# Kernel tuning notes

Measured on AMD Instinct MI355X. Metric: run time of the kernel, lower is better.

Reference implementation:

```python
import jax, jax.numpy as jnp
import numpy as np

L, B = 1024, 64
VALID_FRAC = 0.9  # fraction of residues with nonzero (observed) coordinates in y


def setup_inputs() -> dict:
    key = jax.random.key(0)
    kx, ky = jax.random.split(key)
    x = jax.random.normal(kx, (L, B, 3), dtype=jnp.float32)
    y = jax.random.normal(ky, (L, B, 3), dtype=jnp.float32)
    # zero out trailing residues in y so the dynamic mask (co.sum() != 0) is exercised
    valid = (jnp.arange(L) < int(VALID_FRAC * L))[:, None, None]
    y = y * valid.astype(jnp.float32)
    return {"x": x, "y": y}


def _masked_pair_dist(pts, pair_mask):
    # pts: [B, L, 3]; pair_mask: [B, L, L] (False on diagonal and on padded rows/cols)
    sq = jnp.sum(pts * pts, axis=-1)                                   # [B, L]
    d2 = sq[:, :, None] + sq[:, None, :] - 2.0 * jnp.einsum('bld,bmd->blm', pts, pts)
    d2 = jnp.maximum(d2, 0.0)                                          # relu, matches F.relu
    safe = jnp.where(pair_mask, d2, 1.0)                               # keep sqrt grad finite
    return jnp.where(pair_mask, jnp.sqrt(safe), 0.0)


def reference(x, y):
    # x, y: [L, B, 3] -> permute to [B, L, 3] as in the torch module
    xb = jnp.transpose(x, (1, 0, 2))
    yb = jnp.transpose(y, (1, 0, 2))
    Bn, Ln = xb.shape[0], xb.shape[1]
    # mask: residues of y whose coordinate sum is nonzero (index_select in original)
    mask = (jnp.sum(yb, axis=-1) != 0)                                 # [B, L]
    off_diag = ~jnp.eye(Ln, dtype=bool)
    pair_mask = mask[:, :, None] & mask[:, None, :] & off_diag         # [B, L, L]
    xd = _masked_pair_dist(xb, pair_mask)
    yd = _masked_pair_dist(yb, pair_mask)
    D = yd - xd                                                        # [B, L, L]
    per_batch = jnp.sqrt(jnp.sum(D * D, axis=(1, 2)))                  # Frobenius norm per batch
    denom = (Ln ** 2 / 2 - Ln) ** 0.5                                  # x.size(1)**2/2 - x.size(1)
    out = jnp.sum(per_batch) / denom / Bn
    return out.reshape(1)
```

## Files before the change

### kernel.cpp

```cpp
#include <hip/hip_runtime.h>
#include <math.h>

#define Lp 1024
#define Bp 64
#define Tt 128
#define NTILE 8
#define NPAIR 36

typedef float v2 __attribute__((ext_vector_type(2)));
static __device__ __forceinline__ v2 splat2(float s) { v2 r; r.x = s; r.y = s; return r; }
static __device__ __forceinline__ v2 lo2(float4 v)   { v2 r; r.x = v.x; r.y = v.y; return r; }
static __device__ __forceinline__ v2 hi2(float4 v)   { v2 r; r.x = v.z; r.y = v.w; return r; }

__global__ __launch_bounds__(256) void drmsd_main(
    const float* __restrict__ x, const float* __restrict__ y,
    float* __restrict__ partials, float* __restrict__ moments)
{
    __shared__ __align__(16) float xsx[2][Tt], xsy[2][Tt], xsz[2][Tt];
    __shared__ __align__(16) float ysx[2][Tt], ysy[2][Tt], ysz[2][Tt];
    __shared__ __align__(16) float ms[2][Tt];
    __shared__ float red[4];
    __shared__ float mred[4][9];

    const int b = blockIdx.x;
    const int p = blockIdx.y;
    const int t = threadIdx.x;

    int ti = 0, base = 0;
    while (p >= base + (NTILE - ti)) { base += (NTILE - ti); ++ti; }
    const int tj = ti + (p - base);

    {
        const int r     = t & (Tt - 1);
        const int which = t >> 7;
        const int tile  = which ? tj : ti;
        const int row   = tile * Tt + r;
        const float* px = x + (size_t)row * (Bp * 3) + (size_t)b * 3;
        const float* py = y + (size_t)row * (Bp * 3) + (size_t)b * 3;
        const float x0 = px[0], x1 = px[1], x2 = px[2];
        const float y0 = py[0], y1 = py[1], y2 = py[2];
        xsx[which][r] = x0; xsy[which][r] = x1; xsz[which][r] = x2;
        ysx[which][r] = y0; ysy[which][r] = y1; ysz[which][r] = y2;
        ms[which][r]  = ((y0 + y1 + y2) != 0.0f) ? 1.0f : 0.0f;
    }
    __syncthreads();

    const int jc = (t & 15) << 2;
    const int rg = t >> 4;

    float4 jxx[2], jxy[2], jxz[2], jyx[2], jyy[2], jyz[2], jm4[2];
#pragma unroll
    for (int jj = 0; jj < 2; ++jj) {
        const int j0 = jj * 64 + jc;
        jxx[jj] = *(const float4*)&xsx[1][j0];
        jxy[jj] = *(const float4*)&xsy[1][j0];
        jxz[jj] = *(const float4*)&xsz[1][j0];
        jyx[jj] = *(const float4*)&ysx[1][j0];
        jyy[jj] = *(const float4*)&ysy[1][j0];
        jyz[jj] = *(const float4*)&ysz[1][j0];
        jm4[jj] = *(const float4*)&ms[1][j0];
    }

    float total = 0.0f;

#pragma unroll
    for (int half = 0; half < 2; ++half) {
        const int i0 = half * 64 + rg * 4;
        const float4 v_xx = *(const float4*)&xsx[0][i0];
        const float4 v_xy = *(const float4*)&xsy[0][i0];
        const float4 v_xz = *(const float4*)&xsz[0][i0];
        const float4 v_yx = *(const float4*)&ysx[0][i0];
        const float4 v_yy = *(const float4*)&ysy[0][i0];
        const float4 v_yz = *(const float4*)&ysz[0][i0];
        const float4 v_mi = *(const float4*)&ms[0][i0];
        const float xix[4] = { v_xx.x, v_xx.y, v_xx.z, v_xx.w };
        const float xiy[4] = { v_xy.x, v_xy.y, v_xy.z, v_xy.w };
        const float xiz[4] = { v_xz.x, v_xz.y, v_xz.z, v_xz.w };
        const float yix[4] = { v_yx.x, v_yx.y, v_yx.z, v_yx.w };
        const float yiy[4] = { v_yy.x, v_yy.y, v_yy.z, v_yy.w };
        const float yiz[4] = { v_yz.x, v_yz.y, v_yz.z, v_yz.w };
        const float mir[4] = { v_mi.x, v_mi.y, v_mi.z, v_mi.w };

        v2 acc[4];
#pragma unroll
        for (int r = 0; r < 4; ++r) acc[r] = splat2(0.0f);

#pragma unroll
        for (int jj = 0; jj < 2; ++jj) {
#pragma unroll
            for (int s = 0; s < 2; ++s) {
                const v2 xjx = s ? hi2(jxx[jj]) : lo2(jxx[jj]);
                const v2 xjy = s ? hi2(jxy[jj]) : lo2(jxy[jj]);
                const v2 xjz = s ? hi2(jxz[jj]) : lo2(jxz[jj]);
                const v2 yjx = s ? hi2(jyx[jj]) : lo2(jyx[jj]);
                const v2 yjy = s ? hi2(jyy[jj]) : lo2(jyy[jj]);
                const v2 yjz = s ? hi2(jyz[jj]) : lo2(jyz[jj]);
                const v2 mj  = s ? hi2(jm4[jj]) : lo2(jm4[jj]);
#pragma unroll
                for (int r = 0; r < 4; ++r) {
                    const v2 ax = splat2(xix[r]) - xjx;
                    const v2 ay = splat2(xiy[r]) - xjy;
                    const v2 az = splat2(xiz[r]) - xjz;
                    const v2 d2x = ax * ax + ay * ay + az * az;
                    const v2 bx = splat2(yix[r]) - yjx;
                    const v2 by = splat2(yiy[r]) - yjy;
                    const v2 bz = splat2(yiz[r]) - yjz;
                    const v2 d2y = bx * bx + by * by + bz * bz;
                    const v2 pr = d2x * d2y;
                    v2 sq;
                    sq.x = __builtin_amdgcn_sqrtf(pr.x);
                    sq.y = __builtin_amdgcn_sqrtf(pr.y);
                    acc[r] = mj * sq + acc[r];
                }
            }
        }
#pragma unroll
        for (int r = 0; r < 4; ++r)
            total = fmaf(acc[r].x + acc[r].y, mir[r], total);
    }

#pragma unroll
    for (int off = 32; off > 0; off >>= 1)
        total += __shfl_down(total, off, 64);
    const int wave = t >> 6;
    if ((t & 63) == 0) red[wave] = total;
    __syncthreads();
    if (t == 0) {
        float s = red[0] + red[1] + red[2] + red[3];
        if (ti != tj) s *= 2.0f;
        partials[(size_t)p * Bp + b] = s;
    }

    if (ti == tj) {
        float v[9];
#pragma unroll
        for (int k = 0; k < 9; ++k) v[k] = 0.0f;
        if (t < Tt) {
            const float x0 = xsx[0][t], x1 = xsy[0][t], x2 = xsz[0][t];
            const float y0 = ysx[0][t], y1 = ysy[0][t], y2 = ysz[0][t];
            const float m  = ms[0][t];
            v[0] = m * x0; v[1] = m * x1; v[2] = m * x2;
            v[3] = m * fmaf(x0, x0, fmaf(x1, x1, x2 * x2));
            v[4] = m * y0; v[5] = m * y1; v[6] = m * y2;
            v[7] = m * fmaf(y0, y0, fmaf(y1, y1, y2 * y2));
            v[8] = m;
        }
#pragma unroll
        for (int k = 0; k < 9; ++k) {
#pragma unroll
            for (int off = 32; off > 0; off >>= 1)
                v[k] += __shfl_down(v[k], off, 64);
        }
        if ((t & 63) == 0) {
#pragma unroll
            for (int k = 0; k < 9; ++k) mred[wave][k] = v[k];
        }
        __syncthreads();
        if (t < 9)
            moments[(size_t)(ti * 9 + t) * Bp + b] =
                mred[0][t] + mred[1][t] + mred[2][t] + mred[3][t];
    }
}

__global__ __launch_bounds__(64) void drmsd_final(
    const float* __restrict__ partials, const float* __restrict__ moments,
    float* __restrict__ out)
{
    const int b = threadIdx.x;
    double cross = 0.0;
#pragma unroll
    for (int pp = 0; pp < NPAIR; ++pp)
        cross += (double)partials[(size_t)pp * Bp + b];

    double mo[9];
#pragma unroll
    for (int k = 0; k < 9; ++k) mo[k] = 0.0;
#pragma unroll
    for (int s = 0; s < NTILE; ++s) {
#pragma unroll
        for (int k = 0; k < 9; ++k)
            mo[k] += (double)moments[(size_t)(s * 9 + k) * Bp + b];
    }
    const double sx0 = mo[0], sx1 = mo[1], sx2 = mo[2], qx = mo[3];
    const double sy0 = mo[4], sy1 = mo[5], sy2 = mo[6], qy = mo[7];
    const double M   = mo[8];
    const double term1 = 2.0 * M * (qx + qy)
        - 2.0 * (sx0*sx0 + sx1*sx1 + sx2*sx2 + sy0*sy0 + sy1*sy1 + sy2*sy2);

    double su = term1 - 2.0 * cross;
    su = su > 0.0 ? su : 0.0;
    double pb = sqrt(su);
#pragma unroll
    for (int off = 32; off > 0; off >>= 1)
        pb += __shfl_down(pb, off, 64);
    if (b == 0) {
        const double denom = sqrt((double)Lp * (double)Lp / 2.0 - (double)Lp);
        out[0] = (float)(pb / denom / (double)Bp);
    }
}

extern "C" void kernel_launch(void* const* d_in, const int* in_sizes, int n_in,
                              void* d_out, int out_size, void* d_ws, size_t ws_size,
                              hipStream_t stream) {
    const float* x = (const float*)d_in[0];
    const float* y = (const float*)d_in[1];
    float* out      = (float*)d_out;
    float* partials = (float*)d_ws;
    float* moments  = partials + NPAIR * Bp;

    dim3 grid(Bp, NPAIR);
    drmsd_main<<<grid, 256, 0, stream>>>(x, y, partials, moments);
    drmsd_final<<<1, 64, 0, stream>>>(partials, moments, out);
}
```

Measured before the change: 71.62 us.

## Process two batches per block with two waves each and wider vector loads

Each block now handles two batch elements, with two waves assigned to each batch. The grid shrinks to half as many blocks, and each thread covers four row groups instead of two. Coordinates for both batches are loaded with contiguous float2 loads in place of scalar loads, which improves coalescing. The change also adds an occupancy hint to the launch bounds. Per-thread work per block doubles, which cuts block count and lowers the ratio of load overhead to compute, at the cost of less parallelism across blocks (1152 blocks).

```diff
diff --git a/kernel.cpp b/kernel.cpp
--- a/kernel.cpp
+++ b/kernel.cpp
@@ -6,96 +6,102 @@
 #define Tt 128
 #define NTILE 8
 #define NPAIR 36
+#define BPB 2
 
 typedef float v2 __attribute__((ext_vector_type(2)));
 static __device__ __forceinline__ v2 splat2(float s) { v2 r; r.x = s; r.y = s; return r; }
 static __device__ __forceinline__ v2 lo2(float4 v)   { v2 r; r.x = v.x; r.y = v.y; return r; }
 static __device__ __forceinline__ v2 hi2(float4 v)   { v2 r; r.x = v.z; r.y = v.w; return r; }
 
-__global__ __launch_bounds__(256) void drmsd_main(
+__global__ __launch_bounds__(256, 4) void drmsd_main(
     const float* __restrict__ x, const float* __restrict__ y,
     float* __restrict__ partials, float* __restrict__ moments)
 {
-    __shared__ __align__(16) float xsx[2][Tt], xsy[2][Tt], xsz[2][Tt];
-    __shared__ __align__(16) float ysx[2][Tt], ysy[2][Tt], ysz[2][Tt];
-    __shared__ __align__(16) float ms[2][Tt];
+    __shared__ __align__(16) float xs[2][3][BPB][Tt];
+    __shared__ __align__(16) float ys[2][3][BPB][Tt];
+    __shared__ __align__(16) float msk[2][BPB][Tt];
     __shared__ float red[4];
     __shared__ float mred[4][9];
 
-    const int b = blockIdx.x;
-    const int p = blockIdx.y;
-    const int t = threadIdx.x;
+    const int b0 = blockIdx.x * BPB;
+    const int p  = blockIdx.y;
+    const int t  = threadIdx.x;
 
     int ti = 0, base = 0;
     while (p >= base + (NTILE - ti)) { base += (NTILE - ti); ++ti; }
     const int tj = ti + (p - base);
 
     {
+        const int which = t >> 7;
         const int r     = t & (Tt - 1);
-        const int which = t >> 7;
         const int tile  = which ? tj : ti;
         const int row   = tile * Tt + r;
-        const float* px = x + (size_t)row * (Bp * 3) + (size_t)b * 3;
-        const float* py = y + (size_t)row * (Bp * 3) + (size_t)b * 3;
-        const float x0 = px[0], x1 = px[1], x2 = px[2];
-        const float y0 = py[0], y1 = py[1], y2 = py[2];
-        xsx[which][r] = x0; xsy[which][r] = x1; xsz[which][r] = x2;
-        ysx[which][r] = y0; ysy[which][r] = y1; ysz[which][r] = y2;
-        ms[which][r]  = ((y0 + y1 + y2) != 0.0f) ? 1.0f : 0.0f;
+        const float* px = x + (size_t)row * (Bp * 3) + (size_t)b0 * 3;
+        const float* py = y + (size_t)row * (Bp * 3) + (size_t)b0 * 3;
+        const float2 xa = *(const float2*)(px + 0);
+        const float2 xb = *(const float2*)(px + 2);
+        const float2 xc = *(const float2*)(px + 4);
+        const float2 ya = *(const float2*)(py + 0);
+        const float2 yb = *(const float2*)(py + 2);
+        const float2 yc = *(const float2*)(py + 4);
+        xs[which][0][0][r] = xa.x; xs[which][1][0][r] = xa.y; xs[which][2][0][r] = xb.x;
+        xs[which][0][1][r] = xb.y; xs[which][1][1][r] = xc.x; xs[which][2][1][r] = xc.y;
+        ys[which][0][0][r] = ya.x; ys[which][1][0][r] = ya.y; ys[which][2][0][r] = yb.x;
+        ys[which][0][1][r] = yb.y; ys[which][1][1][r] = yc.x; ys[which][2][1][r] = yc.y;
+        msk[which][0][r] = ((ya.x + ya.y + yb.x) != 0.0f) ? 1.0f : 0.0f;
+        msk[which][1][r] = ((yb.y + yc.x + yc.y) != 0.0f) ? 1.0f : 0.0f;
     }
     __syncthreads();
 
-    const int jc = (t & 15) << 2;
-    const int rg = t >> 4;
-
-    float4 jxx[2], jxy[2], jxz[2], jyx[2], jyy[2], jyz[2], jm4[2];
+    const int wv = t >> 6;
+    const int wb = wv >> 1;
+    const int tp = (t & 63) | ((wv & 1) << 6);
+    const int rg = tp >> 4;
+    const int jc = (tp & 15) << 2;
+
+    float total = 0.0f;
+
 #pragma unroll
     for (int jj = 0; jj < 2; ++jj) {
         const int j0 = jj * 64 + jc;
-        jxx[jj] = *(const float4*)&xsx[1][j0];
-        jxy[jj] = *(const float4*)&xsy[1][j0];
-        jxz[jj] = *(const float4*)&xsz[1][j0];
-        jyx[jj] = *(const float4*)&ysx[1][j0];
-        jyy[jj] = *(const float4*)&ysy[1][j0];
-        jyz[jj] = *(const float4*)&ysz[1][j0];
-        jm4[jj] = *(const float4*)&ms[1][j0];
-    }
-
-    float total = 0.0f;
-
-#pragma unroll
-    for (int half = 0; half < 2; ++half) {
-        const int i0 = half * 64 + rg * 4;
-        const float4 v_xx = *(const float4*)&xsx[0][i0];
-        const float4 v_xy = *(const float4*)&xsy[0][i0];
-        const float4 v_xz = *(const float4*)&xsz[0][i0];
-        const float4 v_yx = *(const float4*)&ysx[0][i0];
-        const float4 v_yy = *(const float4*)&ysy[0][i0];
-        const float4 v_yz = *(const float4*)&ysz[0][i0];
-        const float4 v_mi = *(const float4*)&ms[0][i0];
-        const float xix[4] = { v_xx.x, v_xx.y, v_xx.z, v_xx.w };
-        const float xiy[4] = { v_xy.x, v_xy.y, v_xy.z, v_xy.w };
-        const float xiz[4] = { v_xz.x, v_xz.y, v_xz.z, v_xz.w };
-        const float yix[4] = { v_yx.x, v_yx.y, v_yx.z, v_yx.w };
-        const float yiy[4] = { v_yy.x, v_yy.y, v_yy.z, v_yy.w };
-        const float yiz[4] = { v_yz.x, v_yz.y, v_yz.z, v_yz.w };
-        const float mir[4] = { v_mi.x, v_mi.y, v_mi.z, v_mi.w };
-
-        v2 acc[4];
-#pragma unroll
-        for (int r = 0; r < 4; ++r) acc[r] = splat2(0.0f);
-
-#pragma unroll
-        for (int jj = 0; jj < 2; ++jj) {
+        const float4 jx0 = *(const float4*)&xs[1][0][wb][j0];
+        const float4 jx1 = *(const float4*)&xs[1][1][wb][j0];
+        const float4 jx2 = *(const float4*)&xs[1][2][wb][j0];
+        const float4 jy0 = *(const float4*)&ys[1][0][wb][j0];
+        const float4 jy1 = *(const float4*)&ys[1][1][wb][j0];
+        const float4 jy2 = *(const float4*)&ys[1][2][wb][j0];
+        const float4 jm4 = *(const float4*)&msk[1][wb][j0];
+#pragma unroll
+        for (int q = 0; q < 4; ++q) {
+            const int i0 = q * 32 + rg * 4;
+            const float4 ix0 = *(const float4*)&xs[0][0][wb][i0];
+            const float4 ix1 = *(const float4*)&xs[0][1][wb][i0];
+            const float4 ix2 = *(const float4*)&xs[0][2][wb][i0];
+            const float4 iy0 = *(const float4*)&ys[0][0][wb][i0];
+            const float4 iy1 = *(const float4*)&ys[0][1][wb][i0];
+            const float4 iy2 = *(const float4*)&ys[0][2][wb][i0];
+            const float4 im4 = *(const float4*)&msk[0][wb][i0];
+            const float xix[4] = { ix0.x, ix0.y, ix0.z, ix0.w };
+            const float xiy[4] = { ix1.x, ix1.y, ix1.z, ix1.w };
+            const float xiz[4] = { ix2.x, ix2.y, ix2.z, ix2.w };
+            const float yix[4] = { iy0.x, iy0.y, iy0.z, iy0.w };
+            const float yiy[4] = { iy1.x, iy1.y, iy1.z, iy1.w };
+            const float yiz[4] = { iy2.x, iy2.y, iy2.z, iy2.w };
+            const float mir[4] = { im4.x, im4.y, im4.z, im4.w };
+
+            v2 acc[4];
+#pragma unroll
+            for (int r = 0; r < 4; ++r) acc[r] = splat2(0.0f);
+
 #pragma unroll
             for (int s = 0; s < 2; ++s) {
-                const v2 xjx = s ? hi2(jxx[jj]) : lo2(jxx[jj]);
-                const v2 xjy = s ? hi2(jxy[jj]) : lo2(jxy[jj]);
-                const v2 xjz = s ? hi2(jxz[jj]) : lo2(jxz[jj]);
-                const v2 yjx = s ? hi2(jyx[jj]) : lo2(jyx[jj]);
-                const v2 yjy = s ? hi2(jyy[jj]) : lo2(jyy[jj]);
-                const v2 yjz = s ? hi2(jyz[jj]) : lo2(jyz[jj]);
-                const v2 mj  = s ? hi2(jm4[jj]) : lo2(jm4[jj]);
+                const v2 xjx = s ? hi2(jx0) : lo2(jx0);
+                const v2 xjy = s ? hi2(jx1) : lo2(jx1);
+                const v2 xjz = s ? hi2(jx2) : lo2(jx2);
+                const v2 yjx = s ? hi2(jy0) : lo2(jy0);
+                const v2 yjy = s ? hi2(jy1) : lo2(jy1);
+                const v2 yjz = s ? hi2(jy2) : lo2(jy2);
+                const v2 mj  = s ? hi2(jm4) : lo2(jm4);
 #pragma unroll
                 for (int r = 0; r < 4; ++r) {
                     const v2 ax = splat2(xix[r]) - xjx;
@@ -113,32 +119,33 @@
                     acc[r] = mj * sq + acc[r];
                 }
             }
-        }
-#pragma unroll
-        for (int r = 0; r < 4; ++r)
-            total = fmaf(acc[r].x + acc[r].y, mir[r], total);
+#pragma unroll
+            for (int r = 0; r < 4; ++r)
+                total = fmaf(acc[r].x + acc[r].y, mir[r], total);
+        }
     }
 
 #pragma unroll
     for (int off = 32; off > 0; off >>= 1)
         total += __shfl_down(total, off, 64);
-    const int wave = t >> 6;
-    if ((t & 63) == 0) red[wave] = total;
+    if ((t & 63) == 0) red[wv] = total;
     __syncthreads();
     if (t == 0) {
-        float s = red[0] + red[1] + red[2] + red[3];
-        if (ti != tj) s *= 2.0f;
-        partials[(size_t)p * Bp + b] = s;
+        float s0 = red[0] + red[1];
+        float s1 = red[2] + red[3];
+        if (ti != tj) { s0 *= 2.0f; s1 *= 2.0f; }
+        partials[(size_t)p * Bp + b0]     = s0;
+        partials[(size_t)p * Bp + b0 + 1] = s1;
     }
 
     if (ti == tj) {
+        const int l    = t & 63;
+        const int rrow = ((wv & 1) << 6) | l;
         float v[9];
-#pragma unroll
-        for (int k = 0; k < 9; ++k) v[k] = 0.0f;
-        if (t < Tt) {
-            const float x0 = xsx[0][t], x1 = xsy[0][t], x2 = xsz[0][t];
-            const float y0 = ysx[0][t], y1 = ysy[0][t], y2 = ysz[0][t];
-            const float m  = ms[0][t];
+        {
+            const float x0 = xs[0][0][wb][rrow], x1 = xs[0][1][wb][rrow], x2 = xs[0][2][wb][rrow];
+            const float y0 = ys[0][0][wb][rrow], y1 = ys[0][1][wb][rrow], y2 = ys[0][2][wb][rrow];
+            const float m  = msk[0][wb][rrow];
             v[0] = m * x0; v[1] = m * x1; v[2] = m * x2;
             v[3] = m * fmaf(x0, x0, fmaf(x1, x1, x2 * x2));
             v[4] = m * y0; v[5] = m * y1; v[6] = m * y2;
@@ -151,14 +158,16 @@
             for (int off = 32; off > 0; off >>= 1)
                 v[k] += __shfl_down(v[k], off, 64);
         }
-        if ((t & 63) == 0) {
-#pragma unroll
-            for (int k = 0; k < 9; ++k) mred[wave][k] = v[k];
+        if (l == 0) {
+#pragma unroll
+            for (int k = 0; k < 9; ++k) mred[wv][k] = v[k];
         }
         __syncthreads();
         if (t < 9)
-            moments[(size_t)(ti * 9 + t) * Bp + b] =
-                mred[0][t] + mred[1][t] + mred[2][t] + mred[3][t];
+            moments[(size_t)(ti * 9 + t) * Bp + b0] = mred[0][t] + mred[1][t];
+        else if (t >= 64 && t < 73)
+            moments[(size_t)(ti * 9 + (t - 64)) * Bp + b0 + 1] =
+                mred[2][t - 64] + mred[3][t - 64];
     }
 }
 
@@ -208,7 +217,7 @@
     float* partials = (float*)d_ws;
     float* moments  = partials + NPAIR * Bp;
 
-    dim3 grid(Bp, NPAIR);
+    dim3 grid(Bp / BPB, NPAIR);
     drmsd_main<<<grid, 256, 0, stream>>>(x, y, partials, moments);
     drmsd_final<<<1, 64, 0, stream>>>(partials, moments, out);
 }
```

Result: slower. 131.6 us (+83.8%).
